# Performance work log

Hardware: AMD Instinct MI355X
Metric: run time of the kernel (lower is better)

## Reference

```python
import jax, jax.numpy as jnp
import numpy as np

B, N, M, C, H = 131072, 6, 3, 2, 64
DT, ALPHA, BETA, KAPPA = 0.01, 0.5, 2.0, 0.0
NOISE_EPS = 1e-7


def setup_inputs() -> dict:
    key = jax.random.key(0)
    ks = jax.random.split(key, 7)
    x = jax.random.normal(ks[0], (B, N), dtype=jnp.float32)
    A = 0.1 * jax.random.normal(ks[1], (B, N, N), dtype=jnp.float32)
    # PD covariance so the (single) Cholesky succeeds, matching the torch happy path
    P = jnp.einsum('bij,bkj->bik', A, A) + 0.1 * jnp.eye(N, dtype=jnp.float32)
    u = jax.random.normal(ks[2], (B, C), dtype=jnp.float32)
    y = jax.random.normal(ks[3], (B, M), dtype=jnp.float32)
    LQ = 0.1 * jnp.eye(N, dtype=jnp.float32)
    LR = 0.1 * jnp.eye(M, dtype=jnp.float32)
    W1 = 0.1 * jax.random.normal(ks[4], (N + C, H), dtype=jnp.float32)
    b1 = jnp.zeros((H,), jnp.float32)
    W2 = 0.1 * jax.random.normal(ks[5], (H, N), dtype=jnp.float32)
    b2 = jnp.zeros((N,), jnp.float32)
    return dict(x=x, P=P, u=u, y=y, LQ=LQ, LR=LR, W1=W1, b1=b1, W2=W2, b2=b2)


def _dynamics(x, u, W1, b1, W2, b2):
    # learned vehicle dynamics: MLP over [state, control]
    h = jnp.tanh(jnp.concatenate([x, u], axis=-1) @ W1 + b1)
    return h @ W2 + b2


def _rk4_step(x, u, dt, params):
    k1 = _dynamics(x, u, *params)
    k2 = _dynamics(x + dt / 2.0 * k1, u, *params)
    k3 = _dynamics(x + dt / 2.0 * k2, u, *params)
    k4 = _dynamics(x + dt * k3, u, *params)
    return x + dt / 6.0 * (k1 + 2 * k2 + 2 * k3 + k4)


def _ukf_forward(x, P, u, y, LQ, LR, W1, b1, W2, b2):
    n, m = N, M
    lam = ALPHA ** 2 * (n + KAPPA) - n
    I_n = jnp.eye(n, dtype=x.dtype)
    I_m = jnp.eye(m, dtype=x.dtype)

    # --- sigma points (vectorized over all 2n+1 points) ---
    P_sym = 0.5 * (P + jnp.swapaxes(P, -1, -2))
    base = (n + lam) * P_sym + 1e-5 * I_n
    sqrt_P = jnp.linalg.cholesky(base)                       # (B, n, n)
    cols = jnp.swapaxes(sqrt_P, -1, -2)                      # (B, n, n), cols[:, i] = i-th column
    sigma = jnp.concatenate(
        [x[:, None, :], x[:, None, :] + cols, x[:, None, :] - cols], axis=1
    )                                                         # (B, 2n+1, n)
    S_pts = 2 * n + 1
    w = 1.0 / (2.0 * (n + lam))
    Wm = jnp.full((S_pts,), w, dtype=x.dtype).at[0].set(lam / (n + lam))
    Wc = jnp.full((S_pts,), w, dtype=x.dtype).at[0].set(lam / (n + lam) + (1 - ALPHA ** 2 + BETA))

    # --- propagate all sigma points through RK4 at once ---
    params = (W1, b1, W2, b2)
    u_b = jnp.broadcast_to(u[:, None, :], (x.shape[0], S_pts, C))
    sigma_pred = _rk4_step(sigma, u_b, DT, params)            # (B, 2n+1, n)

    x_pred = jnp.einsum('s,bsi->bi', Wm, sigma_pred)
    dx = sigma_pred - x_pred[:, None, :]
    LQt = jnp.tril(LQ)
    Q = LQt @ LQt.T + NOISE_EPS * I_n
    P_pred = jnp.einsum('s,bsi,bsj->bij', Wc, dx, dx) + Q

    # --- measurement: first m states ---
    sigma_meas = sigma_pred[..., :m]                          # (B, 2n+1, m)
    y_pred = jnp.einsum('s,bsi->bi', Wm, sigma_meas)
    dy = sigma_meas - y_pred[:, None, :]
    LRt = jnp.tril(LR)
    R = LRt @ LRt.T + NOISE_EPS * I_m
    S = jnp.einsum('s,bsi,bsj->bij', Wc, dy, dy) + R
    cross = jnp.einsum('s,bsi,bsj->bij', Wc, dx, dy)

    S_inv = jnp.linalg.inv(S + 1e-5 * I_m)
    K = cross @ S_inv                                         # (B, n, m)
    innov = y - y_pred
    x_updated = x_pred + jnp.einsum('bij,bj->bi', K, innov)
    P_updated = P_pred - K @ S @ jnp.swapaxes(K, -1, -2)
    P_updated = 0.5 * (P_updated + jnp.swapaxes(P_updated, -1, -2)) + 1e-4 * I_n
    return x_updated, P_updated, x_pred, P_pred, y_pred, S, K


def reference(x, P, u, y, LQ, LR, W1, b1, W2, b2):
    return _ukf_forward(x, P, u, y, LQ, LR, W1, b1, W2, b2)
```

## Files before the change

### kernel.cpp

```cpp
#include <hip/hip_runtime.h>
#include <math.h>

typedef __attribute__((ext_vector_type(8)))  short bf16x8;
typedef __attribute__((ext_vector_type(4)))  float f32x4;
typedef __attribute__((ext_vector_type(16))) float f32x16;
typedef __attribute__((ext_vector_type(2)))  float f32x2;

#define TRI(i,j) (((i)*((i)+1))/2 + (j))
#define ONE3 0.3333333333333333f
#define QOFF 6144
#define LOFF 8192

static __device__ __forceinline__ unsigned short f2b(float f) {
  union { float f; unsigned u; } v; v.f = f;
  unsigned r = v.u + 0x7FFFu + ((v.u >> 16) & 1u);
  return (unsigned short)(r >> 16);
}
static __device__ __forceinline__ unsigned pk2(float lo, float hi) {
  return (unsigned)f2b(lo) | ((unsigned)f2b(hi) << 16);
}
static __device__ __forceinline__ unsigned pk2t(float lo, float hi) {
  return __builtin_amdgcn_perm(__float_as_uint(hi), __float_as_uint(lo), 0x07060302u);
}

#define TC0 0.970866f
#define TC1 (-0.217815f)
#define TC2 0.028904f
#define TC3 (-0.0014079f)

static __device__ __forceinline__ unsigned tanh2_pk(float a, float b) {
#if __has_builtin(__builtin_elementwise_fma)
  f32x2 z; z[0] = a; z[1] = b;
  f32x2 k3 = {TC3, TC3}, k2 = {TC2, TC2}, k1 = {TC1, TC1}, k0 = {TC0, TC0};
  f32x2 t = z * z;
  f32x2 p = __builtin_elementwise_fma(t, k3, k2);
  p = __builtin_elementwise_fma(p, t, k1);
  p = __builtin_elementwise_fma(p, t, k0);
  f32x2 r = z * p;
  return pk2t(r[0], r[1]);
#else
  float ta = a * a, tb = b * b;
  float pa = fmaf(fmaf(fmaf(TC3, ta, TC2), ta, TC1), ta, TC0);
  float pb = fmaf(fmaf(fmaf(TC3, tb, TC2), tb, TC1), tb, TC0);
  return pk2t(a * pa, b * pb);
#endif
}

__global__ void prep_kernel(const float* __restrict__ gP,
                            const float* __restrict__ W1, const float* __restrict__ b1,
                            const float* __restrict__ W2,
                            const float* __restrict__ LQ, const float* __restrict__ LR,
                            char* __restrict__ ws, float* __restrict__ Lbuf, int B) {
  if (blockIdx.x == 0 && threadIdx.x < 64) {
    int lane = threadIdx.x;
    int mr = lane & 31, u = lane >> 5;
    unsigned* A1 = (unsigned*)(ws + lane * 96);
    unsigned* A2 = (unsigned*)(ws + lane * 96 + 32);
#pragma unroll
    for (int t = 0; t < 2; ++t) {
      int h = 32 * t + mr;
      if (u == 0) {
#pragma unroll
        for (int p = 0; p < 4; ++p)
          A1[t * 4 + p] = pk2(W1[(2 * p) * 64 + h], W1[(2 * p + 1) * 64 + h]);
      } else {
        A1[t * 4 + 0] = pk2(b1[h], 0.0f);
        A1[t * 4 + 1] = 0u; A1[t * 4 + 2] = 0u; A1[t * 4 + 3] = 0u;
      }
    }
#pragma unroll
    for (int kq = 0; kq < 4; ++kq) {
#pragma unroll
      for (int p = 0; p < 4; ++p) {
        int rm = 2 * p + ((p >= 2) ? 4 : 0);
        int hid = 32 * (kq >> 1) + 16 * (kq & 1) + 4 * u + rm;
        float lo = (mr < 6) ? W2[hid * 6 + mr] : 0.0f;
        float hi = (mr < 6) ? W2[(hid + 1) * 6 + mr] : 0.0f;
        A2[kq * 4 + p] = pk2(lo, hi);
      }
    }
    if (lane == 0) {
      float* qo = (float*)(ws + QOFF);
      for (int i = 0; i < 6; ++i)
        for (int j = 0; j <= i; ++j) {
          float s = (i == j) ? 1e-7f : 0.0f;
          for (int k = 0; k <= j; ++k) s = fmaf(LQ[i * 6 + k], LQ[j * 6 + k], s);
          qo[TRI(i, j)] = s;
        }
      for (int i = 0; i < 3; ++i)
        for (int j = 0; j <= i; ++j) {
          float s = (i == j) ? 1e-7f : 0.0f;
          for (int k = 0; k <= j; ++k) s = fmaf(LR[i * 3 + k], LR[j * 3 + k], s);
          qo[21 + TRI(i, j)] = s;
        }
    }
  }

  int b = blockIdx.x * blockDim.x + threadIdx.x;
  if (b >= B) return;
  float Pf[36];
  const float4* p4 = (const float4*)(gP + (size_t)b * 36);
#pragma unroll
  for (int q = 0; q < 9; ++q) {
    float4 v = p4[q];
    Pf[q*4+0]=v.x; Pf[q*4+1]=v.y; Pf[q*4+2]=v.z; Pf[q*4+3]=v.w;
  }
  float base[21], Lt[21];
#pragma unroll
  for (int i = 0; i < 6; ++i)
#pragma unroll
    for (int j = 0; j <= i; ++j)
      base[TRI(i,j)] = 0.75f * (Pf[i*6+j] + Pf[j*6+i]) + ((i==j) ? 1e-5f : 0.0f);
#pragma unroll
  for (int k = 0; k < 6; ++k) {
    float s = base[TRI(k,k)];
#pragma unroll
    for (int m2 = 0; m2 < k; ++m2) s = fmaf(-Lt[TRI(k,m2)], Lt[TRI(k,m2)], s);
    float d = sqrtf(s);
    Lt[TRI(k,k)] = d;
    float inv = 1.0f / d;
#pragma unroll
    for (int i = k + 1; i < 6; ++i) {
      float s2 = base[TRI(i,k)];
#pragma unroll
      for (int m2 = 0; m2 < k; ++m2) s2 = fmaf(-Lt[TRI(i,m2)], Lt[TRI(k,m2)], s2);
      Lt[TRI(i,k)] = s2 * inv;
    }
  }
  float* lp = Lbuf + (size_t)b * 40;
#pragma unroll
  for (int c = 0; c < 6; ++c)
#pragma unroll
    for (int f = 0; f < 6; ++f)
      lp[c * 6 + f] = (f >= c) ? Lt[TRI(f, c)] : 0.0f;
}

__launch_bounds__(256, 4)
__global__ void ukf_main(const float* __restrict__ gx,
                         const float* __restrict__ gu,
                         const float* __restrict__ gb2,
                         const float* __restrict__ Lbuf,
                         const char*  __restrict__ ws,
                         float* __restrict__ Ubuf, int B) {
  __shared__ f32x4 ldsv[4][136];
  int lane = threadIdx.x & 63;
  int wid  = threadIdx.x >> 6;
  int p    = blockIdx.x * 4 + wid;
  if (2 * p >= B) return;
  int u   = lane >> 5;
  int c   = lane & 31;
  int q16 = lane >> 4, m16 = lane & 15;
  int bc  = 2 * p + ((lane >> 4) & 1);
  float* dxs = (float*)&ldsv[wid][0];

  int   sidx = c & 15;
  float sgn = (sidx == 0 || sidx > 12) ? 0.0f : ((sidx <= 6) ? 1.0f : -1.0f);
  int   cc  = (sidx >= 1 && sidx <= 6) ? (sidx - 1) : ((sidx >= 7) ? (sidx - 7) : 0);
  if (cc > 5) cc = 5;
  const float* lpr = Lbuf + (size_t)bc * 40 + cc * 6;
  float Lc[6];
#pragma unroll
  for (int f = 0; f < 6; ++f) Lc[f] = lpr[f];

  float x0c[6];
  {
    const float* xb = gx + (size_t)bc * 6;
    float2 t0 = *(const float2*)(xb);
    float2 t1 = *(const float2*)(xb + 2);
    float2 t2 = *(const float2*)(xb + 4);
    x0c[0]=t0.x; x0c[1]=t0.y; x0c[2]=t1.x; x0c[3]=t1.y; x0c[4]=t2.x; x0c[5]=t2.y;
  }
  float2 uu = *(const float2*)(gu + (size_t)bc * 2);
  unsigned uu_pk = pk2(uu.x, uu.y);

  const char* wp = ws + lane * 96;
  bf16x8 A1v0 = *((const bf16x8*)wp);
  bf16x8 A1v1 = *((const bf16x8*)(wp + 16));
  bf16x8 A2v[4];
#pragma unroll
  for (int kq = 0; kq < 4; ++kq) A2v[kq] = *((const bf16x8*)(wp + 32 + kq * 16));
  float b2r[6];
#pragma unroll
  for (int i = 0; i < 6; ++i) b2r[i] = gb2[i];

  float xs[6], sgnLp[6], xs005[6];
#pragma unroll
  for (int f = 0; f < 6; ++f) {
    float sl = sgn * Lc[f];
    xs[f] = x0c[f] + sl;
    sgnLp[f] = fmaf(0.01f, b2r[f], sl);
  }
  union { bf16x8 v; unsigned w[4]; } bx;
  bx.w[0] = u ? 0x00003F80u : pk2t(xs[0], xs[1]);
  bx.w[1] = pk2t(xs[2], xs[3]);
  bx.w[2] = pk2t(xs[4], xs[5]);
  bx.w[3] = uu_pk;
#pragma unroll
  for (int f = 0; f < 6; ++f) xs005[f] = fmaf(0.005f, b2r[f], xs[f]);

  f32x16 z16;
#pragma unroll
  for (int i = 0; i < 16; ++i) z16[i] = 0.0f;

  float ksum[4] = {0.f, 0.f, 0.f, 0.f};
#pragma unroll
  for (int st = 0; st < 4; ++st) {
    f32x16 d1a = __builtin_amdgcn_mfma_f32_32x32x16_bf16(A1v0, bx.v, z16, 0, 0, 0);
    f32x16 d1b = __builtin_amdgcn_mfma_f32_32x32x16_bf16(A1v1, bx.v, z16, 0, 0, 0);
    unsigned Hpk[16];
#pragma unroll
    for (int pr = 0; pr < 8; ++pr) Hpk[pr]     = tanh2_pk(d1a[2*pr], d1a[2*pr+1]);
#pragma unroll
    for (int pr = 0; pr < 8; ++pr) Hpk[8 + pr] = tanh2_pk(d1b[2*pr], d1b[2*pr+1]);
    f32x16 d2 = z16;
#pragma unroll
    for (int kq = 0; kq < 4; ++kq) {
      union { bf16x8 v; unsigned w[4]; } bh;
      bh.w[0] = Hpk[4*kq+0]; bh.w[1] = Hpk[4*kq+1];
      bh.w[2] = Hpk[4*kq+2]; bh.w[3] = Hpk[4*kq+3];
      d2 = __builtin_amdgcn_mfma_f32_32x32x16_bf16(A2v[kq], bh.v, d2, 0, 0, 0);
    }
    const float wks = (st == 0 || st == 3) ? 1.0f : 2.0f;
#pragma unroll
    for (int g = 0; g < 4; ++g) ksum[g] = fmaf(wks, d2[g], ksum[g]);
    if (st < 3) {
      float e0 = __shfl_xor(d2[0], 32, 64);
      float e1 = __shfl_xor(d2[1], 32, 64);
      float e2 = __shfl_xor(d2[2], 32, 64);
      float e3 = __shfl_xor(d2[3], 32, 64);
      float k0 = u ? e0 : d2[0];
      float k1 = u ? e1 : d2[1];
      float k2 = u ? e2 : d2[2];
      float k3 = u ? e3 : d2[3];
      float k4 = u ? d2[0] : e0;
      float k5 = u ? d2[1] : e1;
      const float cin = (st == 2) ? 0.01f : 0.005f;
      float base0, base1, base2, base3, base4, base5;
      if (st == 2) {
        base0 = fmaf(0.005f, b2r[0], xs005[0]); base1 = fmaf(0.005f, b2r[1], xs005[1]);
        base2 = fmaf(0.005f, b2r[2], xs005[2]); base3 = fmaf(0.005f, b2r[3], xs005[3]);
        base4 = fmaf(0.005f, b2r[4], xs005[4]); base5 = fmaf(0.005f, b2r[5], xs005[5]);
      } else {
        base0 = xs005[0]; base1 = xs005[1]; base2 = xs005[2];
        base3 = xs005[3]; base4 = xs005[4]; base5 = xs005[5];
      }
      float xi0 = fmaf(cin, k0, base0), xi1 = fmaf(cin, k1, base1);
      float xi2 = fmaf(cin, k2, base2), xi3 = fmaf(cin, k3, base3);
      float xi4 = fmaf(cin, k4, base4), xi5 = fmaf(cin, k5, base5);
      bx.w[0] = u ? 0x00003F80u : pk2t(xi0, xi1);
      bx.w[1] = pk2t(xi2, xi3);
      bx.w[2] = pk2t(xi4, xi5);
    }
  }

  const float dt6 = 0.01f / 6.0f;
  if (u == 0) {
#pragma unroll
    for (int g = 0; g < 4; ++g) dxs[c * 17 + g] = fmaf(dt6, ksum[g], sgnLp[g]);
  } else {
#pragma unroll
    for (int g = 0; g < 2; ++g) dxs[c * 17 + 4 + g] = fmaf(dt6, ksum[g], sgnLp[4 + g]);
  }

  float dxv[8];
#pragma unroll
  for (int j = 0; j < 8; ++j) dxv[j] = dxs[(8 * q16 + j) * 17 + m16];
  float wc0[8], wc1[8];
#pragma unroll
  for (int j = 0; j < 8; ++j) {
    float c0j = (j == 0) ? -0.25f : ONE3;
    float c1j = (j <= 4) ? ONE3 : 0.0f;
    wc0[j] = (q16 == 0) ? c0j : ((q16 == 1) ? c1j : 0.0f);
    wc1[j] = (q16 == 2) ? c0j : ((q16 == 3) ? c1j : 0.0f);
  }
  float wm00 = (q16 == 0) ? -3.0f : wc0[0];
  float wm10 = (q16 == 2) ? -3.0f : wc1[0];
  bool mlt6 = (m16 < 6), m6 = (m16 == 6), m7 = (m16 == 7);
  union { bf16x8 v; unsigned w[4]; } am0, am1, bw;
  {
    float a0[8], a1[8];
#pragma unroll
    for (int j = 0; j < 8; ++j) {
      float wmj0 = (j == 0) ? wm00 : wc0[j];
      float wmj1 = (j == 0) ? wm10 : wc1[j];
      float alt0 = m6 ? wc0[j] : (m7 ? wmj0 : 0.0f);
      float alt1 = m6 ? wc1[j] : (m7 ? wmj1 : 0.0f);
      a0[j] = mlt6 ? wc0[j] * dxv[j] : alt0;
      a1[j] = mlt6 ? wc1[j] * dxv[j] : alt1;
    }
#pragma unroll
    for (int pr = 0; pr < 4; ++pr) {
      am0.w[pr] = pk2(a0[2*pr], a0[2*pr+1]);
      am1.w[pr] = pk2(a1[2*pr], a1[2*pr+1]);
      bw.w[pr]  = pk2(dxv[2*pr], dxv[2*pr+1]);
    }
  }
  f32x4 zz = {0.0f, 0.0f, 0.0f, 0.0f};
  f32x4 Dm0 = __builtin_amdgcn_mfma_f32_16x16x32_bf16(am0.v, bw.v, zz, 0, 0, 0);
  f32x4 Dm1 = __builtin_amdgcn_mfma_f32_16x16x32_bf16(am1.v, bw.v, zz, 0, 0, 0);

  if (q16 < 2 && m16 < 6) {
    float* u0 = Ubuf + (size_t)(2 * p) * 48;
    float* u1 = Ubuf + (size_t)(2 * p + 1) * 48;
#pragma unroll
    for (int i = 0; i < 4; ++i) {
      u0[(4 * q16 + i) * 6 + m16] = Dm0[i];
      u1[(4 * q16 + i) * 6 + m16] = Dm1[i];
    }
  }
}

__global__ void ukf_epi(const float* __restrict__ gx,
                        const float* __restrict__ gy,
                        const char*  __restrict__ ws,
                        const float* __restrict__ Ubuf,
                        float* __restrict__ out, int B) {
  int b = blockIdx.x * blockDim.x + threadIdx.x;
  if (b >= B) return;
  const float* rec = Ubuf + (size_t)b * 48;
  float U[21], cbv[6], dbv[6];
#pragma unroll
  for (int i = 0; i < 6; ++i)
#pragma unroll
    for (int j = 0; j <= i; ++j) U[TRI(i,j)] = rec[i * 6 + j];
#pragma unroll
  for (int j = 0; j < 6; ++j) { cbv[j] = rec[36 + j]; dbv[j] = rec[42 + j]; }

  float x0[6];
  {
    const float* xb = gx + (size_t)b * 6;
    float2 t0 = *(const float2*)(xb);
    float2 t1 = *(const float2*)(xb + 2);
    float2 t2 = *(const float2*)(xb + 4);
    x0[0]=t0.x; x0[1]=t0.y; x0[2]=t1.x; x0[3]=t1.y; x0[4]=t2.x; x0[5]=t2.y;
  }
  const float* yb = gy + (size_t)b * 3;
  float yy0 = yb[0], yy1 = yb[1], yy2 = yb[2];

  const float* qro = (const float*)(ws + QOFF);
  float Qm[21], Rm[6];
#pragma unroll
  for (int t = 0; t < 21; ++t) Qm[t] = qro[t];
#pragma unroll
  for (int t = 0; t < 6; ++t) Rm[t] = qro[21 + t];

  float xp[6];
#pragma unroll
  for (int i = 0; i < 6; ++i) xp[i] = x0[i] + dbv[i];
  float D[21];
#pragma unroll
  for (int i = 0; i < 6; ++i)
#pragma unroll
    for (int j = 0; j <= i; ++j) {
      float v = U[TRI(i,j)];
      v -= cbv[i] * dbv[j];
      v -= dbv[i] * cbv[j];
      v = fmaf(3.75f * dbv[i], dbv[j], v);
      D[TRI(i,j)] = v;
    }
  float s00 = D[TRI(0,0)] + Rm[TRI(0,0)];
  float s10 = D[TRI(1,0)] + Rm[TRI(1,0)];
  float s11 = D[TRI(1,1)] + Rm[TRI(1,1)];
  float s20 = D[TRI(2,0)] + Rm[TRI(2,0)];
  float s21 = D[TRI(2,1)] + Rm[TRI(2,1)];
  float s22 = D[TRI(2,2)] + Rm[TRI(2,2)];
  float a00 = s00 + 1e-5f, a11 = s11 + 1e-5f, a22 = s22 + 1e-5f;
  float a10 = s10, a20 = s20, a21 = s21;
  float adj00 = a11*a22 - a21*a21;
  float adj01 = a20*a21 - a10*a22;
  float adj02 = a10*a21 - a11*a20;
  float adj11 = a00*a22 - a20*a20;
  float adj12 = a10*a20 - a00*a21;
  float adj22 = a00*a11 - a10*a10;
  float det  = a00*adj00 + a10*adj01 + a20*adj02;
  float idet = 1.0f / det;
  float I00 = adj00*idet, I01 = adj01*idet, I02 = adj02*idet;
  float I11 = adj11*idet, I12 = adj12*idet, I22 = adj22*idet;

#define DS(i,j) ((i) >= (j) ? D[TRI(i,j)] : D[TRI(j,i)])
  float K_[18];
#pragma unroll
  for (int i = 0; i < 6; ++i) {
    float c0 = DS(i,0), c1 = DS(i,1), c2 = DS(i,2);
    K_[i*3+0] = c0*I00 + c1*I01 + c2*I02;
    K_[i*3+1] = c0*I01 + c1*I11 + c2*I12;
    K_[i*3+2] = c0*I02 + c1*I12 + c2*I22;
  }
  float inn0 = yy0 - xp[0], inn1 = yy1 - xp[1], inn2 = yy2 - xp[2];
  float xu[6];
#pragma unroll
  for (int i = 0; i < 6; ++i)
    xu[i] = xp[i] + K_[i*3]*inn0 + K_[i*3+1]*inn1 + K_[i*3+2]*inn2;

  float KS[18];
#pragma unroll
  for (int i = 0; i < 6; ++i) {
    float k0 = K_[i*3], k1 = K_[i*3+1], k2 = K_[i*3+2];
    KS[i*3+0] = k0*s00 + k1*s10 + k2*s20;
    KS[i*3+1] = k0*s10 + k1*s11 + k2*s21;
    KS[i*3+2] = k0*s20 + k1*s21 + k2*s22;
  }
  float Pu[21];
#pragma unroll
  for (int i = 0; i < 6; ++i)
#pragma unroll
    for (int j = 0; j <= i; ++j) {
      float v = D[TRI(i,j)] + Qm[TRI(i,j)];
      v -= KS[i*3]*K_[j*3] + KS[i*3+1]*K_[j*3+1] + KS[i*3+2]*K_[j*3+2];
      Pu[TRI(i,j)] = v + ((i==j) ? 1e-4f : 0.0f);
    }

  float* o_xu = out;
  float* o_Pu = out + (size_t)6  * B;
  float* o_xp = out + (size_t)42 * B;
  float* o_Pp = out + (size_t)48 * B;
  float* o_yp = out + (size_t)84 * B;
  float* o_S  = out + (size_t)87 * B;
  float* o_K  = out + (size_t)96 * B;
  {
    float* pp = o_xu + (size_t)b * 6;
    ((float2*)pp)[0] = make_float2(xu[0], xu[1]);
    ((float2*)pp)[1] = make_float2(xu[2], xu[3]);
    ((float2*)pp)[2] = make_float2(xu[4], xu[5]);
  }
  {
    float* pp = o_Pu + (size_t)b * 36;
#pragma unroll
    for (int i = 0; i < 6; ++i)
#pragma unroll
      for (int j = 0; j < 6; j += 2) {
        float v0 = (i>=j)   ? Pu[TRI(i,j)]   : Pu[TRI(j,i)];
        float v1 = (i>=j+1) ? Pu[TRI(i,j+1)] : Pu[TRI(j+1,i)];
        *(float2*)(pp + i*6 + j) = make_float2(v0, v1);
      }
  }
  {
    float* pp = o_xp + (size_t)b * 6;
    ((float2*)pp)[0] = make_float2(xp[0], xp[1]);
    ((float2*)pp)[1] = make_float2(xp[2], xp[3]);
    ((float2*)pp)[2] = make_float2(xp[4], xp[5]);
  }
  {
    float* pp = o_Pp + (size_t)b * 36;
#pragma unroll
    for (int i = 0; i < 6; ++i)
#pragma unroll
      for (int j = 0; j < 6; j += 2) {
        float v0 = ((i>=j)   ? D[TRI(i,j)]   : D[TRI(j,i)])   + ((i>=j)   ? Qm[TRI(i,j)]   : Qm[TRI(j,i)]);
        float v1 = ((i>=j+1) ? D[TRI(i,j+1)] : D[TRI(j+1,i)]) + ((i>=j+1) ? Qm[TRI(i,j+1)] : Qm[TRI(j+1,i)]);
        *(float2*)(pp + i*6 + j) = make_float2(v0, v1);
      }
  }
  {
    float* pp = o_yp + (size_t)b * 3;
    pp[0] = xp[0]; pp[1] = xp[1]; pp[2] = xp[2];
  }
  {
    float* pp = o_S + (size_t)b * 9;
    pp[0]=s00; pp[1]=s10; pp[2]=s20;
    pp[3]=s10; pp[4]=s11; pp[5]=s21;
    pp[6]=s20; pp[7]=s21; pp[8]=s22;
  }
  {
    float* pp = o_K + (size_t)b * 18;
#pragma unroll
    for (int i = 0; i < 9; ++i)
      ((float2*)pp)[i] = make_float2(K_[i*2], K_[i*2+1]);
  }
}

extern "C" void kernel_launch(void* const* d_in, const int* in_sizes, int n_in,
                              void* d_out, int out_size, void* d_ws, size_t ws_size,
                              hipStream_t stream) {
  const float* x  = (const float*)d_in[0];
  const float* P  = (const float*)d_in[1];
  const float* u  = (const float*)d_in[2];
  const float* y  = (const float*)d_in[3];
  const float* LQ = (const float*)d_in[4];
  const float* LR = (const float*)d_in[5];
  const float* W1 = (const float*)d_in[6];
  const float* b1 = (const float*)d_in[7];
  const float* W2 = (const float*)d_in[8];
  const float* b2 = (const float*)d_in[9];
  float* out = (float*)d_out;
  char*  ws  = (char*)d_ws;
  int B = in_sizes[0] / 6;

  float* Lbuf = (float*)(ws + LOFF);
  float* Ubuf = (float*)(ws + LOFF + (size_t)B * 160);

  hipLaunchKernelGGL(prep_kernel, dim3((B + 255) / 256), dim3(256), 0, stream,
                     P, W1, b1, W2, LQ, LR, ws, Lbuf, B);
  hipLaunchKernelGGL(ukf_main, dim3((B + 7) / 8), dim3(256), 0, stream,
                     x, u, b2, (const float*)Lbuf, (const char*)ws, Ubuf, B);
  hipLaunchKernelGGL(ukf_epi, dim3((B + 255) / 256), dim3(256), 0, stream,
                     x, y, (const char*)ws, (const float*)Ubuf, out, B);
}
```

Before: 234.3 us.

## Permute W2 output rows so each lane holds all six derivative components

Remaps the W2 A-operand rows so the second MFMA writes all six state derivatives into one lane's accumulator registers. The per-stage cross-half shuffles and selects in the RK4 loop go away. The Cholesky buffer is padded to 8-float rows so it can be read with vector loads. Launch bounds are raised to 8 blocks per CU for more occupancy, at the cost of tighter register limits and possible spills.

After: 444.5 us. 89.7% more time.

```diff
diff --git a/kernel.cpp b/kernel.cpp
--- a/kernel.cpp
+++ b/kernel.cpp
@@ -68,14 +68,17 @@
         A1[t * 4 + 1] = 0u; A1[t * 4 + 2] = 0u; A1[t * 4 + 3] = 0u;
       }
     }
+    int fr = (mr < 4) ? mr
+           : (mr < 10) ? (mr - 4)
+           : (mr >= 12 && mr < 14) ? (mr - 8) : -1;
 #pragma unroll
     for (int kq = 0; kq < 4; ++kq) {
 #pragma unroll
       for (int p = 0; p < 4; ++p) {
         int rm = 2 * p + ((p >= 2) ? 4 : 0);
         int hid = 32 * (kq >> 1) + 16 * (kq & 1) + 4 * u + rm;
-        float lo = (mr < 6) ? W2[hid * 6 + mr] : 0.0f;
-        float hi = (mr < 6) ? W2[(hid + 1) * 6 + mr] : 0.0f;
+        float lo = (fr >= 0) ? W2[hid * 6 + fr] : 0.0f;
+        float hi = (fr >= 0) ? W2[(hid + 1) * 6 + fr] : 0.0f;
         A2[kq * 4 + p] = pk2(lo, hi);
       }
     }
@@ -127,15 +130,17 @@
       Lt[TRI(i,k)] = s2 * inv;
     }
   }
-  float* lp = Lbuf + (size_t)b * 40;
-#pragma unroll
-  for (int c = 0; c < 6; ++c)
+  float* lp = Lbuf + (size_t)b * 48;
+#pragma unroll
+  for (int c = 0; c < 6; ++c) {
 #pragma unroll
     for (int f = 0; f < 6; ++f)
-      lp[c * 6 + f] = (f >= c) ? Lt[TRI(f, c)] : 0.0f;
-}
-
-__launch_bounds__(256, 4)
+      lp[c * 8 + f] = (f >= c) ? Lt[TRI(f, c)] : 0.0f;
+    lp[c * 8 + 6] = 0.0f; lp[c * 8 + 7] = 0.0f;
+  }
+}
+
+__launch_bounds__(256, 8)
 __global__ void ukf_main(const float* __restrict__ gx,
                          const float* __restrict__ gu,
                          const float* __restrict__ gb2,
@@ -157,10 +162,10 @@
   float sgn = (sidx == 0 || sidx > 12) ? 0.0f : ((sidx <= 6) ? 1.0f : -1.0f);
   int   cc  = (sidx >= 1 && sidx <= 6) ? (sidx - 1) : ((sidx >= 7) ? (sidx - 7) : 0);
   if (cc > 5) cc = 5;
-  const float* lpr = Lbuf + (size_t)bc * 40 + cc * 6;
-  float Lc[6];
-#pragma unroll
-  for (int f = 0; f < 6; ++f) Lc[f] = lpr[f];
+  const float* lpr = Lbuf + (size_t)bc * 48 + cc * 8;
+  float4 La = *(const float4*)lpr;
+  float2 Lb = *(const float2*)(lpr + 4);
+  float Lc[6] = {La.x, La.y, La.z, La.w, Lb.x, Lb.y};
 
   float x0c[6];
   {
@@ -202,7 +207,7 @@
 #pragma unroll
   for (int i = 0; i < 16; ++i) z16[i] = 0.0f;
 
-  float ksum[4] = {0.f, 0.f, 0.f, 0.f};
+  float ksum[6] = {0.f, 0.f, 0.f, 0.f, 0.f, 0.f};
 #pragma unroll
   for (int st = 0; st < 4; ++st) {
     f32x16 d1a = __builtin_amdgcn_mfma_f32_32x32x16_bf16(A1v0, bx.v, z16, 0, 0, 0);
@@ -222,44 +227,25 @@
     }
     const float wks = (st == 0 || st == 3) ? 1.0f : 2.0f;
 #pragma unroll
-    for (int g = 0; g < 4; ++g) ksum[g] = fmaf(wks, d2[g], ksum[g]);
+    for (int f = 0; f < 6; ++f) ksum[f] = fmaf(wks, d2[f], ksum[f]);
     if (st < 3) {
-      float e0 = __shfl_xor(d2[0], 32, 64);
-      float e1 = __shfl_xor(d2[1], 32, 64);
-      float e2 = __shfl_xor(d2[2], 32, 64);
-      float e3 = __shfl_xor(d2[3], 32, 64);
-      float k0 = u ? e0 : d2[0];
-      float k1 = u ? e1 : d2[1];
-      float k2 = u ? e2 : d2[2];
-      float k3 = u ? e3 : d2[3];
-      float k4 = u ? d2[0] : e0;
-      float k5 = u ? d2[1] : e1;
       const float cin = (st == 2) ? 0.01f : 0.005f;
-      float base0, base1, base2, base3, base4, base5;
-      if (st == 2) {
-        base0 = fmaf(0.005f, b2r[0], xs005[0]); base1 = fmaf(0.005f, b2r[1], xs005[1]);
-        base2 = fmaf(0.005f, b2r[2], xs005[2]); base3 = fmaf(0.005f, b2r[3], xs005[3]);
-        base4 = fmaf(0.005f, b2r[4], xs005[4]); base5 = fmaf(0.005f, b2r[5], xs005[5]);
-      } else {
-        base0 = xs005[0]; base1 = xs005[1]; base2 = xs005[2];
-        base3 = xs005[3]; base4 = xs005[4]; base5 = xs005[5];
+      float xi[6];
+#pragma unroll
+      for (int f = 0; f < 6; ++f) {
+        float basef = (st == 2) ? fmaf(0.005f, b2r[f], xs005[f]) : xs005[f];
+        xi[f] = fmaf(cin, d2[f], basef);
       }
-      float xi0 = fmaf(cin, k0, base0), xi1 = fmaf(cin, k1, base1);
-      float xi2 = fmaf(cin, k2, base2), xi3 = fmaf(cin, k3, base3);
-      float xi4 = fmaf(cin, k4, base4), xi5 = fmaf(cin, k5, base5);
-      bx.w[0] = u ? 0x00003F80u : pk2t(xi0, xi1);
-      bx.w[1] = pk2t(xi2, xi3);
-      bx.w[2] = pk2t(xi4, xi5);
+      bx.w[0] = u ? 0x00003F80u : pk2t(xi[0], xi[1]);
+      bx.w[1] = pk2t(xi[2], xi[3]);
+      bx.w[2] = pk2t(xi[4], xi[5]);
     }
   }
 
   const float dt6 = 0.01f / 6.0f;
   if (u == 0) {
 #pragma unroll
-    for (int g = 0; g < 4; ++g) dxs[c * 17 + g] = fmaf(dt6, ksum[g], sgnLp[g]);
-  } else {
-#pragma unroll
-    for (int g = 0; g < 2; ++g) dxs[c * 17 + 4 + g] = fmaf(dt6, ksum[g], sgnLp[4 + g]);
+    for (int f = 0; f < 6; ++f) dxs[c * 17 + f] = fmaf(dt6, ksum[f], sgnLp[f]);
   }
 
   float dxv[8];
@@ -487,7 +473,7 @@
   int B = in_sizes[0] / 6;
 
   float* Lbuf = (float*)(ws + LOFF);
-  float* Ubuf = (float*)(ws + LOFF + (size_t)B * 160);
+  float* Ubuf = (float*)(ws + LOFF + (size_t)B * 192);
 
   hipLaunchKernelGGL(prep_kernel, dim3((B + 255) / 256), dim3(256), 0, stream,
                      P, W1, b1, W2, LQ, LR, ws, Lbuf, B);
```
